# Optimization experiments

Measured on AMD Instinct MI355X. Metric: run time of the kernel, lower is better.

## Reference

```python
import jax, jax.numpy as jnp
import numpy as np
from jax import lax

B, C, D, H, W = 2, 64, 20, 20, 20


def _conv3d(x, w, b, pad):
    # x: [B,C,D,H,W], w: [O,I,kd,kh,kw]
    y = lax.conv_general_dilated(
        x, w, window_strides=(1, 1, 1), padding=pad,
        dimension_numbers=('NCDHW', 'OIDHW', 'NCDHW'))
    return y + b[None, :, None, None, None]


def setup_inputs() -> dict:
    key = jax.random.key(0)
    ks = jax.random.split(key, 7)
    s = 1.0 / np.sqrt(C * 3)  # conv fan-in = C*1*3*1
    return {
        'x': jax.random.normal(ks[0], (B, C, D, H, W), jnp.float32),
        'q_w': jax.random.uniform(ks[1], (C, C, 1, 3, 1), jnp.float32, -s, s),
        'q_b': jax.random.uniform(ks[2], (C,), jnp.float32, -s, s),
        'k_w': jax.random.uniform(ks[3], (C, C, 3, 1, 1), jnp.float32, -s, s),
        'k_b': jax.random.uniform(ks[4], (C,), jnp.float32, -s, s),
        'v_w': jax.random.uniform(ks[5], (C, C, 1, 1, 3), jnp.float32, -s, s),
        'v_b': jax.random.uniform(ks[6], (C,), jnp.float32, -s, s),
    }


def reference(x, q_w, q_b, k_w, k_b, v_w, v_b):
    b, c, d, h, w = x.shape
    n = d * h * w
    q0 = _conv3d(x, q_w, q_b, ((0, 0), (1, 1), (0, 0))).reshape(b, c, n)
    k0 = _conv3d(x, k_w, k_b, ((1, 1), (0, 0), (0, 0))).reshape(b, c, n)
    v = _conv3d(x, v_w, v_b, ((0, 0), (0, 0), (1, 1))).reshape(b, c, n)
    # scores[b, i, j] = sum_c k0[b,c,i] * q0[b,c,j]  -> [B, N, N]
    scores = jnp.einsum('bci,bcj->bij', k0, q0)
    # torch Softmax(dim=1) on [B,N,N] normalizes over axis 1 (the i axis)
    attn = jax.nn.softmax(scores, axis=1)
    out = jnp.einsum('bcn,bnm->bcm', v, attn)  # v @ attn
    return out.reshape(b, c, d, h, w)
```

## Files before the change

### kernel.cpp

```cpp
#include <hip/hip_runtime.h>
#include <cstdint>
#include <cstddef>

typedef _Float16 half4_t  __attribute__((ext_vector_type(4)));
typedef _Float16 half8_t  __attribute__((ext_vector_type(8)));
typedef short    short4_t __attribute__((ext_vector_type(4)));
typedef unsigned short ushort4_t __attribute__((ext_vector_type(4)));
typedef float    f32x4_t  __attribute__((ext_vector_type(4)));

#define LOG2E 1.44269504088896340736f

__device__ __forceinline__ float bf2f(unsigned short u) {
    union { unsigned int u; float f; } x;
    x.u = ((unsigned int)u) << 16;
    return x.f;
}
__device__ __forceinline__ unsigned short f2bf(float f) {
    union { float f; unsigned int u; } x;
    x.f = f;
    unsigned int r = (x.u + 0x7FFFu + ((x.u >> 16) & 1u)) >> 16;
    return (unsigned short)r;
}
__device__ __forceinline__ unsigned short f2bf_trunc(float f) {
    union { float f; unsigned int u; } x;
    x.f = f;
    return (unsigned short)(x.u >> 16);
}

__global__ __launch_bounds__(256) void prep_kernel(
    const void* __restrict__ x,
    const void* __restrict__ qw, const void* __restrict__ kw, const void* __restrict__ vw,
    const void* __restrict__ qb, const void* __restrict__ kb, const void* __restrict__ vb,
    int* __restrict__ flag,
    _Float16* __restrict__ w2, float* __restrict__ bb, _Float16* __restrict__ xT)
{
    __shared__ int scnt;
    __shared__ _Float16 tile[64][66];

    if (threadIdx.x == 0) scnt = 0;
    __syncthreads();
    {
        unsigned int w = ((const unsigned int*)x)[threadIdx.x];
        int e = (w >> 7) & 0xFF;
        int hit = (e == 0) || (e >= 0x68 && e <= 0x88);
        atomicAdd(&scnt, hit);
    }
    __syncthreads();
    const int bf = (scnt >= 128) ? 1 : 0;
    if (blockIdx.x == 0 && threadIdx.x == 0) flag[0] = bf;

    if (blockIdx.x < 144) {
        int idx = blockIdx.x * 256 + threadIdx.x;
        if (idx < 36864) {
            int conv = idx / 12288;
            int r    = idx - conv * 12288;
            int tap  = r >> 12;
            int r2   = r & 4095;
            int co   = r2 >> 6;
            int ci   = r2 & 63;
            const void* w = (conv == 0) ? qw : (conv == 1) ? kw : vw;
            float t;
            if (bf) t = bf2f(((const unsigned short*)w)[co * 192 + ci * 3 + tap]);
            else    t = ((const float*)w)[co * 192 + ci * 3 + tap];
            if (conv == 0) t *= LOG2E;
            w2[idx] = (_Float16)t;
        }
        if (idx < 192) {
            int a = idx >> 6, co = idx & 63;
            const void* s = (a == 0) ? qb : (a == 1) ? kb : vb;
            float t = bf ? bf2f(((const unsigned short*)s)[co]) : ((const float*)s)[co];
            if (a == 0) t *= LOG2E;
            bb[idx] = t;
        }
    } else {
        const int bx   = blockIdx.x - 144;
        const int b    = bx / 125;
        const int n0   = (bx - b * 125) * 64;
        const int lane = threadIdx.x & 63;
        const int wv   = threadIdx.x >> 6;

        if (bf) {
            const unsigned short* xb = (const unsigned short*)x + (size_t)b * 512000 + n0 + lane;
#pragma unroll
            for (int i = 0; i < 16; ++i) {
                const int ci = wv * 16 + i;
                tile[ci][lane] = (_Float16)bf2f(xb[(size_t)ci * 8000]);
            }
        } else {
            const float* xb = (const float*)x + (size_t)b * 512000 + n0 + lane;
#pragma unroll
            for (int i = 0; i < 16; ++i) {
                const int ci = wv * 16 + i;
                tile[ci][lane] = (_Float16)xb[(size_t)ci * 8000];
            }
        }
        __syncthreads();
        _Float16* out = xT + ((size_t)b * 8000 + n0) * 64 + lane;
#pragma unroll
        for (int i = 0; i < 16; ++i) {
            const int r = wv * 16 + i;
            out[(size_t)r * 64] = tile[lane][r];
        }
    }
}

__global__ __launch_bounds__(256, 2) void convg_kernel(
    const _Float16* __restrict__ xT, const _Float16* __restrict__ w2,
    const float* __restrict__ bb,
    _Float16* __restrict__ Qt, _Float16* __restrict__ Kt, unsigned short* __restrict__ Vt)
{
    const int tid = threadIdx.x;
    const int wv  = tid >> 6;
    const int L   = tid & 63;
    const int q4  = L >> 4;
    const int lm  = L & 15;
    const int W    = blockIdx.x * 4 + wv;
    const int conv = W % 3;
    const int u    = W / 3;
    const int b    = u / 250;
    const int n0   = (u - b * 250) * 32;

    half8_t wf[3][2][4];
    const _Float16* wbase = w2 + (size_t)conv * 12288;
#pragma unroll
    for (int tap = 0; tap < 3; ++tap)
#pragma unroll
        for (int kh = 0; kh < 2; ++kh)
#pragma unroll
            for (int cb = 0; cb < 4; ++cb)
                wf[tap][kh][cb] = *(const half8_t*)(
                    wbase + ((size_t)(tap * 64 + cb * 16 + lm)) * 64 + kh * 32 + q4 * 8);

    f32x4_t acc[2][4];
#pragma unroll
    for (int cb = 0; cb < 4; ++cb) {
        const float bi = bb[conv * 64 + cb * 16 + lm];
        const f32x4_t v = (f32x4_t){bi, bi, bi, bi};
        acc[0][cb] = v;
        acc[1][cb] = v;
    }

    const _Float16* xb = xT + (size_t)b * 512000;
    const half8_t z8 = {(_Float16)0, (_Float16)0, (_Float16)0, (_Float16)0,
                        (_Float16)0, (_Float16)0, (_Float16)0, (_Float16)0};

#pragma unroll
    for (int mt = 0; mt < 2; ++mt) {
        const int npos = n0 + mt * 16 + lm;
        int gm, gp, off;
        if (conv == 0)      { const int h = (npos / 20) % 20; gm = h > 0; gp = h < 19; off = 20; }
        else if (conv == 1) { const int d = npos / 400;       gm = d > 0; gp = d < 19; off = 400; }
        else                { const int w = npos % 20;        gm = w > 0; gp = w < 19; off = 1; }
        const int rm = gm ? npos - off : npos;
        const int rp = gp ? npos + off : npos;

#pragma unroll
        for (int kh = 0; kh < 2; ++kh) {
            const int ko = kh * 32 + q4 * 8;
            half8_t a0 = *(const half8_t*)(xb + (size_t)rm * 64 + ko);
            const half8_t a1 = *(const half8_t*)(xb + (size_t)npos * 64 + ko);
            half8_t a2 = *(const half8_t*)(xb + (size_t)rp * 64 + ko);
            a0 = gm ? a0 : z8;
            a2 = gp ? a2 : z8;
#pragma unroll
            for (int cb = 0; cb < 4; ++cb) {
                acc[mt][cb] = __builtin_amdgcn_mfma_f32_16x16x32_f16(a0, wf[0][kh][cb], acc[mt][cb], 0, 0, 0);
                acc[mt][cb] = __builtin_amdgcn_mfma_f32_16x16x32_f16(a1, wf[1][kh][cb], acc[mt][cb], 0, 0, 0);
                acc[mt][cb] = __builtin_amdgcn_mfma_f32_16x16x32_f16(a2, wf[2][kh][cb], acc[mt][cb], 0, 0, 0);
            }
        }
    }

    if (conv < 2) {
        _Float16* dst = (conv == 0) ? Qt : Kt;
#pragma unroll
        for (int mt = 0; mt < 2; ++mt)
#pragma unroll
            for (int cb = 0; cb < 4; ++cb)
#pragma unroll
                for (int reg = 0; reg < 4; ++reg) {
                    const int n = n0 + mt * 16 + q4 * 4 + reg;
                    dst[((size_t)b * 8000 + n) * 64 + cb * 16 + lm] = (_Float16)acc[mt][cb][reg];
                }
    } else {
#pragma unroll
        for (int mt = 0; mt < 2; ++mt)
#pragma unroll
            for (int cb = 0; cb < 4; ++cb) {
                ushort4_t vvv;
#pragma unroll
                for (int reg = 0; reg < 4; ++reg) vvv[reg] = f2bf(acc[mt][cb][reg]);
                *(ushort4_t*)(Vt + ((size_t)b * 64 + cb * 16 + lm) * 8000 + n0 + mt * 16 + q4 * 4) = vvv;
            }
    }
}

__global__ __launch_bounds__(256, 4) void attn_kernel(
    const _Float16* __restrict__ Qt, const _Float16* __restrict__ Kt,
    const unsigned short* __restrict__ Vt,
    _Float16* __restrict__ Oseg, float* __restrict__ Wseg)
{
    __shared__ __align__(16) _Float16       k_lds[4096];
    __shared__ __align__(16) unsigned short v_lds[4096];

    const int tid = threadIdx.x;
    const int wv  = tid >> 6;
    const int L   = tid & 63;
    const int q4  = L >> 4;
    const int lm  = L & 15;
    const int qt  = blockIdx.x;
    const int b   = blockIdx.y;
    const int sp  = blockIdx.z;
    const int NS  = gridDim.z;
    const int t0  = (125 * sp) / NS;
    const int t1  = (125 * (sp + 1)) / NS;
    const int unit = qt * 4 + wv;

    const _Float16* Qb = Qt + ((size_t)b * 8000 + (size_t)qt * 128 + wv * 32 + lm) * 64 + q4 * 8;
    half8_t bq00 = *(const half8_t*)(Qb);
    half8_t bq01 = *(const half8_t*)(Qb + 32);
    half8_t bq10 = *(const half8_t*)(Qb + 16 * 64);
    half8_t bq11 = *(const half8_t*)(Qb + 16 * 64 + 32);

    f32x4_t o[2][4];
    f32x4_t acc_l[2];
#pragma unroll
    for (int mt = 0; mt < 2; ++mt) {
        acc_l[mt] = (f32x4_t){0.f, 0.f, 0.f, 0.f};
#pragma unroll
        for (int cb = 0; cb < 4; ++cb) o[mt][cb] = (f32x4_t){0.f, 0.f, 0.f, 0.f};
    }
    const short4_t ones4 = {(short)0x3F80, (short)0x3F80, (short)0x3F80, (short)0x3F80};

    const _Float16*       Kg = Kt + (size_t)b * 512000;
    const unsigned short* Vg = Vt + (size_t)b * 512000;
    const int r0  = tid >> 3;
    const int cc0 = tid & 7;
    const int swz_lo = r0 * 64 + ((cc0 ^ (r0 & 7)) * 8);
    const int swz_hi = (r0 + 32) * 64 + ((cc0 ^ (r0 & 7)) * 8);
    const _Float16*       Kr0 = Kg + (size_t)r0 * 64 + cc0 * 8;
    const _Float16*       Kr1 = Kg + (size_t)(r0 + 32) * 64 + cc0 * 8;
    const unsigned short* Vr0 = Vg + (size_t)r0 * 8000 + cc0 * 8;
    const unsigned short* Vr1 = Vg + (size_t)(r0 + 32) * 8000 + cc0 * 8;

    uint4 sk0, sk1, sv0, sv1;

    {
        const int n0 = t0 * 64;
        sk0 = *(const uint4*)(Kr0 + (size_t)n0 * 64);
        sk1 = *(const uint4*)(Kr1 + (size_t)n0 * 64);
        sv0 = *(const uint4*)(Vr0 + n0);
        sv1 = *(const uint4*)(Vr1 + n0);
    }

    for (int kt = t0; kt < t1; ++kt) {
        __syncthreads();
        *(uint4*)(&k_lds[swz_lo]) = sk0;
        *(uint4*)(&k_lds[swz_hi]) = sk1;
        *(uint4*)(&v_lds[swz_lo]) = sv0;
        *(uint4*)(&v_lds[swz_hi]) = sv1;
        if (kt + 1 < t1) {
            const int n1 = (kt + 1) * 64;
            sk0 = *(const uint4*)(Kr0 + (size_t)n1 * 64);
            sk1 = *(const uint4*)(Kr1 + (size_t)n1 * 64);
            sv0 = *(const uint4*)(Vr0 + n1);
            sv1 = *(const uint4*)(Vr1 + n1);
        }
        __syncthreads();

        short4_t pfr[2][4];
#pragma unroll
        for (int ns = 0; ns < 4; ++ns) {
            const int n = ns * 16 + lm;
            const _Float16* krow = &k_lds[n * 64];
            const half8_t ak0 = *(const half8_t*)(krow + (((q4    ) ^ (n & 7)) * 8));
            const half8_t ak1 = *(const half8_t*)(krow + (((q4 + 4) ^ (n & 7)) * 8));
#pragma unroll
            for (int mt = 0; mt < 2; ++mt) {
                f32x4_t z = (f32x4_t){0.f, 0.f, 0.f, 0.f};
                z = __builtin_amdgcn_mfma_f32_16x16x32_f16(ak0, mt ? bq10 : bq00, z, 0, 0, 0);
                z = __builtin_amdgcn_mfma_f32_16x16x32_f16(ak1, mt ? bq11 : bq01, z, 0, 0, 0);
                short4_t pk;
#pragma unroll
                for (int reg = 0; reg < 4; ++reg)
                    pk[reg] = (short)f2bf_trunc(exp2f(z[reg]));
                pfr[mt][ns] = pk;
            }
        }

#pragma unroll
        for (int mt = 0; mt < 2; ++mt)
#pragma unroll
            for (int ns = 0; ns < 4; ++ns)
                acc_l[mt] = __builtin_amdgcn_mfma_f32_16x16x16bf16_1k(ones4, pfr[mt][ns], acc_l[mt], 0, 0, 0);

#pragma unroll
        for (int cb = 0; cb < 4; ++cb) {
            const int c = cb * 16 + lm;
            const unsigned short* vrow = &v_lds[c * 64];
            f32x4_t a0 = o[0][cb], a1 = o[1][cb];
#pragma unroll
            for (int ns = 0; ns < 4; ++ns) {
                const int cc = ns * 2 + (q4 >> 1);
                const short4_t av = *(const short4_t*)(vrow + ((cc ^ (c & 7)) * 8) + (q4 & 1) * 4);
                a0 = __builtin_amdgcn_mfma_f32_16x16x16bf16_1k(av, pfr[0][ns], a0, 0, 0, 0);
                a1 = __builtin_amdgcn_mfma_f32_16x16x16bf16_1k(av, pfr[1][ns], a1, 0, 0, 0);
            }
            o[0][cb] = a0;
            o[1][cb] = a1;
        }
    }

    if (unit >= 250) return;

    float rinv[2], lv[2];
#pragma unroll
    for (int mt = 0; mt < 2; ++mt) {
        const float l = acc_l[mt][0];
        rinv[mt] = 1.0f / l;
        lv[mt]   = l;
    }

    const int seg = (b * 250 + unit) * NS + sp;
    _Float16* os = Oseg + (size_t)seg * 2048;
#pragma unroll
    for (int mt = 0; mt < 2; ++mt) {
#pragma unroll
        for (int cb = 0; cb < 4; ++cb) {
            half4_t e;
#pragma unroll
            for (int reg = 0; reg < 4; ++reg) e[reg] = (_Float16)(o[mt][cb][reg] * rinv[mt]);
            *(half4_t*)(os + (mt * 16 + lm) * 64 + cb * 16 + q4 * 4) = e;
        }
    }
    if (q4 == 0) {
#pragma unroll
        for (int mt = 0; mt < 2; ++mt)
            Wseg[(size_t)seg * 32 + mt * 16 + lm] = lv[mt];
    }
}

__global__ __launch_bounds__(256, 2) void combine_kernel(
    const _Float16* __restrict__ Oseg, const float* __restrict__ Wseg,
    const int* __restrict__ flag, void* __restrict__ outv, int NS)
{
    __shared__ float cls[8 * 32];
    const int tid = threadIdx.x;
    const int qt = blockIdx.x, b = blockIdx.y;
    const int base = (b * 250 + qt) * NS;

    for (int i = tid; i < NS * 32; i += 256) cls[i] = Wseg[(size_t)base * 32 + i];
    __syncthreads();
    if (tid < 32) {
        const int r = tid;
        float cs = 0.f;
        for (int s2 = 0; s2 < NS; ++s2) cs += cls[s2 * 32 + r];
        const float inv = 1.f / cs;
        for (int s2 = 0; s2 < NS; ++s2) cls[s2 * 32 + r] *= inv;
    }
    __syncthreads();

    const int c = tid & 63, rg = tid >> 6;
    float acc[8];
#pragma unroll
    for (int i = 0; i < 8; ++i) acc[i] = 0.f;
    for (int s2 = 0; s2 < NS; ++s2) {
        const _Float16* src = Oseg + ((size_t)(base + s2)) * 2048 + rg * 8 * 64 + c;
        const float* cf = &cls[s2 * 32 + rg * 8];
#pragma unroll
        for (int i = 0; i < 8; ++i) acc[i] += (float)src[i * 64] * cf[i];
    }

    const size_t ob = ((size_t)b * 64 + c) * 8000 + qt * 32 + rg * 8;
    if (*flag) {
        uint4 u0;
        u0.x = f2bf(acc[0]) | ((unsigned)f2bf(acc[1]) << 16);
        u0.y = f2bf(acc[2]) | ((unsigned)f2bf(acc[3]) << 16);
        u0.z = f2bf(acc[4]) | ((unsigned)f2bf(acc[5]) << 16);
        u0.w = f2bf(acc[6]) | ((unsigned)f2bf(acc[7]) << 16);
        *(uint4*)((unsigned short*)outv + ob) = u0;
    } else {
        float* o32 = (float*)outv + ob;
        *(f32x4_t*)(o32)     = (f32x4_t){acc[0], acc[1], acc[2], acc[3]};
        *(f32x4_t*)(o32 + 4) = (f32x4_t){acc[4], acc[5], acc[6], acc[7]};
    }
}

extern "C" void kernel_launch(void* const* d_in, const int* in_sizes, int n_in,
                              void* d_out, int out_size, void* d_ws, size_t ws_size,
                              hipStream_t stream)
{
    (void)in_sizes; (void)n_in; (void)out_size;
    const void* x  = d_in[0];
    const void* qw = d_in[1];
    const void* qb = d_in[2];
    const void* kw = d_in[3];
    const void* kb = d_in[4];
    const void* vw = d_in[5];
    const void* vb = d_in[6];

    char* ws = (char*)d_ws;
    int*            flag = (int*)ws;
    float*          bb   = (float*)(ws + 2304);
    _Float16*       w2   = (_Float16*)(ws + 3072);
    _Float16*       Qt   = (_Float16*)(ws + 76800);
    _Float16*       Kt   = (_Float16*)(ws + 2124800);
    unsigned short* Vt   = (unsigned short*)(ws + 4172800);
    _Float16*       xT   = (_Float16*)(ws + 6220800);

    const size_t need8 = 6220800 + (size_t)2 * 250 * 8 * 2048 * 2 + (size_t)2 * 250 * 8 * 32 * 4;
    const int NS = (ws_size >= need8) ? 8 : 1;
    _Float16* Oseg = (_Float16*)(ws + 6220800);
    float*    Wseg = (float*)(ws + 6220800 + (size_t)2 * 250 * NS * 2048 * 2);

    prep_kernel<<<dim3(394), 256, 0, stream>>>(x, qw, kw, vw, qb, kb, vb, flag, w2, bb, xT);
    convg_kernel<<<dim3(375), 256, 0, stream>>>(xT, w2, bb, Qt, Kt, Vt);
    attn_kernel<<<dim3(63, 2, NS), 256, 0, stream>>>(Qt, Kt, Vt, Oseg, Wseg);
    combine_kernel<<<dim3(250, 2), 256, 0, stream>>>(Oseg, Wseg, flag, d_out, NS);
}
```

Measured before the change: 143.8 us.

## Fuse four kernel launches into one cooperative persistent kernel with grid syncs

Replaces the four back-to-back launches (prep, conv, attention, combine) with a single cooperative kernel. It loops over work units per phase and separates the phases with grid.sync(). This removes the launch and drain gaps between kernels. The grid size comes from the occupancy query, and the split count NS follows from it, capped at 8. The cost is grid-wide barrier overhead, a possibly different NS than before, and one shared launch-bounds and register budget for every phase. The old four-kernel path stays as a fallback.

```diff
diff --git a/kernel.cpp b/kernel.cpp
--- a/kernel.cpp
+++ b/kernel.cpp
@@ -1,6 +1,9 @@
 #include <hip/hip_runtime.h>
+#include <hip/hip_cooperative_groups.h>
 #include <cstdint>
 #include <cstddef>
+
+namespace cg = cooperative_groups;
 
 typedef _Float16 half4_t  __attribute__((ext_vector_type(4)));
 typedef _Float16 half8_t  __attribute__((ext_vector_type(8)));
@@ -27,6 +30,368 @@
     return (unsigned short)(x.u >> 16);
 }
 
+__global__ __launch_bounds__(256, 4) void mega_kernel(
+    const void* __restrict__ x,
+    const void* __restrict__ qw, const void* __restrict__ kw, const void* __restrict__ vw,
+    const void* __restrict__ qb, const void* __restrict__ kb, const void* __restrict__ vb,
+    _Float16* __restrict__ w2, float* __restrict__ bb, _Float16* __restrict__ xT,
+    _Float16* __restrict__ Qt, _Float16* __restrict__ Kt, unsigned short* __restrict__ Vt,
+    _Float16* __restrict__ Oseg, float* __restrict__ Wseg, void* __restrict__ outv,
+    int NS)
+{
+    __shared__ __align__(16) unsigned char smem[16384];
+    cg::grid_group grid = cg::this_grid();
+    const int nb  = gridDim.x;
+    const int tid = threadIdx.x;
+
+    int* scnt = (int*)(smem + 16380);
+    if (tid == 0) *scnt = 0;
+    __syncthreads();
+    {
+        unsigned int w = ((const unsigned int*)x)[tid];
+        int e = (w >> 7) & 0xFF;
+        int hit = (e == 0) || (e >= 0x68 && e <= 0x88);
+        atomicAdd(scnt, hit);
+    }
+    __syncthreads();
+    const int bf = (*scnt >= 128) ? 1 : 0;
+    __syncthreads();
+
+    for (int u = blockIdx.x; u < 394; u += nb) {
+        if (u < 144) {
+            int idx = u * 256 + tid;
+            if (idx < 36864) {
+                int conv = idx / 12288;
+                int r    = idx - conv * 12288;
+                int tap  = r >> 12;
+                int r2   = r & 4095;
+                int co   = r2 >> 6;
+                int ci   = r2 & 63;
+                const void* w = (conv == 0) ? qw : (conv == 1) ? kw : vw;
+                float t;
+                if (bf) t = bf2f(((const unsigned short*)w)[co * 192 + ci * 3 + tap]);
+                else    t = ((const float*)w)[co * 192 + ci * 3 + tap];
+                if (conv == 0) t *= LOG2E;
+                w2[idx] = (_Float16)t;
+            }
+            if (idx < 192) {
+                int a = idx >> 6, co = idx & 63;
+                const void* s = (a == 0) ? qb : (a == 1) ? kb : vb;
+                float t = bf ? bf2f(((const unsigned short*)s)[co]) : ((const float*)s)[co];
+                if (a == 0) t *= LOG2E;
+                bb[idx] = t;
+            }
+        } else {
+            _Float16 (*tile)[66] = (_Float16 (*)[66])smem;
+            const int bx   = u - 144;
+            const int b    = bx / 125;
+            const int n0   = (bx - b * 125) * 64;
+            const int lane = tid & 63;
+            const int wv   = tid >> 6;
+            if (bf) {
+                const unsigned short* xb = (const unsigned short*)x + (size_t)b * 512000 + n0 + lane;
+#pragma unroll
+                for (int i = 0; i < 16; ++i) {
+                    const int ci = wv * 16 + i;
+                    tile[ci][lane] = (_Float16)bf2f(xb[(size_t)ci * 8000]);
+                }
+            } else {
+                const float* xb = (const float*)x + (size_t)b * 512000 + n0 + lane;
+#pragma unroll
+                for (int i = 0; i < 16; ++i) {
+                    const int ci = wv * 16 + i;
+                    tile[ci][lane] = (_Float16)xb[(size_t)ci * 8000];
+                }
+            }
+            __syncthreads();
+            _Float16* out = xT + ((size_t)b * 8000 + n0) * 64 + lane;
+#pragma unroll
+            for (int i = 0; i < 16; ++i) {
+                const int r = wv * 16 + i;
+                out[(size_t)r * 64] = tile[lane][r];
+            }
+        }
+        __syncthreads();
+    }
+    grid.sync();
+
+    {
+        const int wv = tid >> 6;
+        const int L  = tid & 63;
+        const int q4 = L >> 4;
+        const int lm = L & 15;
+        for (int u = blockIdx.x; u < 375; u += nb) {
+            const int W    = u * 4 + wv;
+            const int conv = W % 3;
+            const int uu   = W / 3;
+            const int b    = uu / 250;
+            const int n0   = (uu - b * 250) * 32;
+
+            f32x4_t acc[2][4];
+#pragma unroll
+            for (int cb = 0; cb < 4; ++cb) {
+                const float bi = bb[conv * 64 + cb * 16 + lm];
+                const f32x4_t v = (f32x4_t){bi, bi, bi, bi};
+                acc[0][cb] = v;
+                acc[1][cb] = v;
+            }
+
+            const _Float16* xb = xT + (size_t)b * 512000;
+            const _Float16* wbase = w2 + (size_t)conv * 12288;
+            const half8_t z8 = {(_Float16)0, (_Float16)0, (_Float16)0, (_Float16)0,
+                                (_Float16)0, (_Float16)0, (_Float16)0, (_Float16)0};
+
+#pragma unroll
+            for (int kh = 0; kh < 2; ++kh) {
+                half8_t wfk[3][4];
+#pragma unroll
+                for (int tap = 0; tap < 3; ++tap)
+#pragma unroll
+                    for (int cb = 0; cb < 4; ++cb)
+                        wfk[tap][cb] = *(const half8_t*)(
+                            wbase + ((size_t)(tap * 64 + cb * 16 + lm)) * 64 + kh * 32 + q4 * 8);
+
+#pragma unroll
+                for (int mt = 0; mt < 2; ++mt) {
+                    const int npos = n0 + mt * 16 + lm;
+                    int gm, gp, off;
+                    if (conv == 0)      { const int h = (npos / 20) % 20; gm = h > 0; gp = h < 19; off = 20; }
+                    else if (conv == 1) { const int d = npos / 400;       gm = d > 0; gp = d < 19; off = 400; }
+                    else                { const int w = npos % 20;        gm = w > 0; gp = w < 19; off = 1; }
+                    const int rm = gm ? npos - off : npos;
+                    const int rp = gp ? npos + off : npos;
+
+                    const int ko = kh * 32 + q4 * 8;
+                    half8_t a0 = *(const half8_t*)(xb + (size_t)rm * 64 + ko);
+                    const half8_t a1 = *(const half8_t*)(xb + (size_t)npos * 64 + ko);
+                    half8_t a2 = *(const half8_t*)(xb + (size_t)rp * 64 + ko);
+                    a0 = gm ? a0 : z8;
+                    a2 = gp ? a2 : z8;
+#pragma unroll
+                    for (int cb = 0; cb < 4; ++cb) {
+                        acc[mt][cb] = __builtin_amdgcn_mfma_f32_16x16x32_f16(a0, wfk[0][cb], acc[mt][cb], 0, 0, 0);
+                        acc[mt][cb] = __builtin_amdgcn_mfma_f32_16x16x32_f16(a1, wfk[1][cb], acc[mt][cb], 0, 0, 0);
+                        acc[mt][cb] = __builtin_amdgcn_mfma_f32_16x16x32_f16(a2, wfk[2][cb], acc[mt][cb], 0, 0, 0);
+                    }
+                }
+            }
+
+            if (conv < 2) {
+                _Float16* dst = (conv == 0) ? Qt : Kt;
+#pragma unroll
+                for (int mt = 0; mt < 2; ++mt)
+#pragma unroll
+                    for (int cb = 0; cb < 4; ++cb)
+#pragma unroll
+                        for (int reg = 0; reg < 4; ++reg) {
+                            const int n = n0 + mt * 16 + q4 * 4 + reg;
+                            dst[((size_t)b * 8000 + n) * 64 + cb * 16 + lm] = (_Float16)acc[mt][cb][reg];
+                        }
+            } else {
+#pragma unroll
+                for (int mt = 0; mt < 2; ++mt)
+#pragma unroll
+                    for (int cb = 0; cb < 4; ++cb) {
+                        ushort4_t vvv;
+#pragma unroll
+                        for (int reg = 0; reg < 4; ++reg) vvv[reg] = f2bf(acc[mt][cb][reg]);
+                        *(ushort4_t*)(Vt + ((size_t)b * 64 + cb * 16 + lm) * 8000 + n0 + mt * 16 + q4 * 4) = vvv;
+                    }
+            }
+        }
+    }
+    grid.sync();
+
+    {
+        _Float16*       k_lds = (_Float16*)smem;
+        unsigned short* v_lds = (unsigned short*)(smem + 8192);
+        const int wv = tid >> 6;
+        const int L  = tid & 63;
+        const int q4 = L >> 4;
+        const int lm = L & 15;
+        const int totalU = 126 * NS;
+
+        for (int bu = blockIdx.x; bu < totalU; bu += nb) {
+            const int sp = bu / 126;
+            const int r  = bu - sp * 126;
+            const int b  = r / 63;
+            const int qt = r - b * 63;
+            const int t0 = (125 * sp) / NS;
+            const int t1 = (125 * (sp + 1)) / NS;
+            const int unit = qt * 4 + wv;
+
+            const _Float16* Qb = Qt + ((size_t)b * 8000 + (size_t)qt * 128 + wv * 32 + lm) * 64 + q4 * 8;
+            half8_t bq00 = *(const half8_t*)(Qb);
+            half8_t bq01 = *(const half8_t*)(Qb + 32);
+            half8_t bq10 = *(const half8_t*)(Qb + 16 * 64);
+            half8_t bq11 = *(const half8_t*)(Qb + 16 * 64 + 32);
+
+            f32x4_t o[2][4];
+            f32x4_t acc_l[2];
+#pragma unroll
+            for (int mt = 0; mt < 2; ++mt) {
+                acc_l[mt] = (f32x4_t){0.f, 0.f, 0.f, 0.f};
+#pragma unroll
+                for (int cb = 0; cb < 4; ++cb) o[mt][cb] = (f32x4_t){0.f, 0.f, 0.f, 0.f};
+            }
+            const short4_t ones4 = {(short)0x3F80, (short)0x3F80, (short)0x3F80, (short)0x3F80};
+
+            const _Float16*       Kg = Kt + (size_t)b * 512000;
+            const unsigned short* Vg = Vt + (size_t)b * 512000;
+            const int r0  = tid >> 3;
+            const int cc0 = tid & 7;
+            const int swz_lo = r0 * 64 + ((cc0 ^ (r0 & 7)) * 8);
+            const int swz_hi = (r0 + 32) * 64 + ((cc0 ^ (r0 & 7)) * 8);
+            const _Float16*       Kr0 = Kg + (size_t)r0 * 64 + cc0 * 8;
+            const _Float16*       Kr1 = Kg + (size_t)(r0 + 32) * 64 + cc0 * 8;
+            const unsigned short* Vr0 = Vg + (size_t)r0 * 8000 + cc0 * 8;
+            const unsigned short* Vr1 = Vg + (size_t)(r0 + 32) * 8000 + cc0 * 8;
+
+            uint4 sk0, sk1, sv0, sv1;
+            {
+                const int n0 = t0 * 64;
+                sk0 = *(const uint4*)(Kr0 + (size_t)n0 * 64);
+                sk1 = *(const uint4*)(Kr1 + (size_t)n0 * 64);
+                sv0 = *(const uint4*)(Vr0 + n0);
+                sv1 = *(const uint4*)(Vr1 + n0);
+            }
+
+            for (int kt = t0; kt < t1; ++kt) {
+                __syncthreads();
+                *(uint4*)(&k_lds[swz_lo]) = sk0;
+                *(uint4*)(&k_lds[swz_hi]) = sk1;
+                *(uint4*)(&v_lds[swz_lo]) = sv0;
+                *(uint4*)(&v_lds[swz_hi]) = sv1;
+                if (kt + 1 < t1) {
+                    const int n1 = (kt + 1) * 64;
+                    sk0 = *(const uint4*)(Kr0 + (size_t)n1 * 64);
+                    sk1 = *(const uint4*)(Kr1 + (size_t)n1 * 64);
+                    sv0 = *(const uint4*)(Vr0 + n1);
+                    sv1 = *(const uint4*)(Vr1 + n1);
+                }
+                __syncthreads();
+
+                short4_t pfr[2][4];
+#pragma unroll
+                for (int ns = 0; ns < 4; ++ns) {
+                    const int n = ns * 16 + lm;
+                    const _Float16* krow = &k_lds[n * 64];
+                    const half8_t ak0 = *(const half8_t*)(krow + (((q4    ) ^ (n & 7)) * 8));
+                    const half8_t ak1 = *(const half8_t*)(krow + (((q4 + 4) ^ (n & 7)) * 8));
+#pragma unroll
+                    for (int mt = 0; mt < 2; ++mt) {
+                        f32x4_t z = (f32x4_t){0.f, 0.f, 0.f, 0.f};
+                        z = __builtin_amdgcn_mfma_f32_16x16x32_f16(ak0, mt ? bq10 : bq00, z, 0, 0, 0);
+                        z = __builtin_amdgcn_mfma_f32_16x16x32_f16(ak1, mt ? bq11 : bq01, z, 0, 0, 0);
+                        short4_t pk;
+#pragma unroll
+                        for (int reg = 0; reg < 4; ++reg)
+                            pk[reg] = (short)f2bf_trunc(exp2f(z[reg]));
+                        pfr[mt][ns] = pk;
+                    }
+                }
+
+#pragma unroll
+                for (int mt = 0; mt < 2; ++mt)
+#pragma unroll
+                    for (int ns = 0; ns < 4; ++ns)
+                        acc_l[mt] = __builtin_amdgcn_mfma_f32_16x16x16bf16_1k(ones4, pfr[mt][ns], acc_l[mt], 0, 0, 0);
+
+#pragma unroll
+                for (int cb = 0; cb < 4; ++cb) {
+                    const int c = cb * 16 + lm;
+                    const unsigned short* vrow = &v_lds[c * 64];
+                    f32x4_t a0 = o[0][cb], a1 = o[1][cb];
+#pragma unroll
+                    for (int ns = 0; ns < 4; ++ns) {
+                        const int cc = ns * 2 + (q4 >> 1);
+                        const short4_t av = *(const short4_t*)(vrow + ((cc ^ (c & 7)) * 8) + (q4 & 1) * 4);
+                        a0 = __builtin_amdgcn_mfma_f32_16x16x16bf16_1k(av, pfr[0][ns], a0, 0, 0, 0);
+                        a1 = __builtin_amdgcn_mfma_f32_16x16x16bf16_1k(av, pfr[1][ns], a1, 0, 0, 0);
+                    }
+                    o[0][cb] = a0;
+                    o[1][cb] = a1;
+                }
+            }
+            __syncthreads();
+
+            if (unit < 250) {
+                float rinv[2], lv[2];
+#pragma unroll
+                for (int mt = 0; mt < 2; ++mt) {
+                    const float l = acc_l[mt][0];
+                    rinv[mt] = 1.0f / l;
+                    lv[mt]   = l;
+                }
+                const int seg = (b * 250 + unit) * NS + sp;
+                _Float16* os = Oseg + (size_t)seg * 2048;
+#pragma unroll
+                for (int mt = 0; mt < 2; ++mt) {
+#pragma unroll
+                    for (int cb = 0; cb < 4; ++cb) {
+                        half4_t e;
+#pragma unroll
+                        for (int reg = 0; reg < 4; ++reg) e[reg] = (_Float16)(o[mt][cb][reg] * rinv[mt]);
+                        *(half4_t*)(os + (mt * 16 + lm) * 64 + cb * 16 + q4 * 4) = e;
+                    }
+                }
+                if (q4 == 0) {
+#pragma unroll
+                    for (int mt = 0; mt < 2; ++mt)
+                        Wseg[(size_t)seg * 32 + mt * 16 + lm] = lv[mt];
+                }
+            }
+        }
+    }
+    grid.sync();
+
+    {
+        float* cls = (float*)smem;
+        for (int v = blockIdx.x; v < 500; v += nb) {
+            const int b  = v / 250;
+            const int qt = v - b * 250;
+            const int base = (b * 250 + qt) * NS;
+
+            for (int i = tid; i < NS * 32; i += 256) cls[i] = Wseg[(size_t)base * 32 + i];
+            __syncthreads();
+            if (tid < 32) {
+                const int r = tid;
+                float cs = 0.f;
+                for (int s2 = 0; s2 < NS; ++s2) cs += cls[s2 * 32 + r];
+                const float inv = 1.f / cs;
+                for (int s2 = 0; s2 < NS; ++s2) cls[s2 * 32 + r] *= inv;
+            }
+            __syncthreads();
+
+            const int c = tid & 63, rg = tid >> 6;
+            float acc[8];
+#pragma unroll
+            for (int i = 0; i < 8; ++i) acc[i] = 0.f;
+            for (int s2 = 0; s2 < NS; ++s2) {
+                const _Float16* src = Oseg + ((size_t)(base + s2)) * 2048 + rg * 8 * 64 + c;
+                const float* cf = &cls[s2 * 32 + rg * 8];
+#pragma unroll
+                for (int i = 0; i < 8; ++i) acc[i] += (float)src[i * 64] * cf[i];
+            }
+
+            const size_t ob = ((size_t)b * 64 + c) * 8000 + qt * 32 + rg * 8;
+            if (bf) {
+                uint4 u0;
+                u0.x = f2bf(acc[0]) | ((unsigned)f2bf(acc[1]) << 16);
+                u0.y = f2bf(acc[2]) | ((unsigned)f2bf(acc[3]) << 16);
+                u0.z = f2bf(acc[4]) | ((unsigned)f2bf(acc[5]) << 16);
+                u0.w = f2bf(acc[6]) | ((unsigned)f2bf(acc[7]) << 16);
+                *(uint4*)((unsigned short*)outv + ob) = u0;
+            } else {
+                float* o32 = (float*)outv + ob;
+                *(f32x4_t*)(o32)     = (f32x4_t){acc[0], acc[1], acc[2], acc[3]};
+                *(f32x4_t*)(o32 + 4) = (f32x4_t){acc[4], acc[5], acc[6], acc[7]};
+            }
+            __syncthreads();
+        }
+    }
+}
+
 __global__ __launch_bounds__(256) void prep_kernel(
     const void* __restrict__ x,
     const void* __restrict__ qw, const void* __restrict__ kw, const void* __restrict__ vw,
@@ -244,7 +609,6 @@
     const unsigned short* Vr1 = Vg + (size_t)(r0 + 32) * 8000 + cc0 * 8;
 
     uint4 sk0, sk1, sv0, sv1;
-
     {
         const int n0 = t0 * 64;
         sk0 = *(const uint4*)(Kr0 + (size_t)n0 * 64);
@@ -408,13 +772,40 @@
     unsigned short* Vt   = (unsigned short*)(ws + 4172800);
     _Float16*       xT   = (_Float16*)(ws + 6220800);
 
-    const size_t need8 = 6220800 + (size_t)2 * 250 * 8 * 2048 * 2 + (size_t)2 * 250 * 8 * 32 * 4;
-    const int NS = (ws_size >= need8) ? 8 : 1;
-    _Float16* Oseg = (_Float16*)(ws + 6220800);
-    float*    Wseg = (float*)(ws + 6220800 + (size_t)2 * 250 * NS * 2048 * 2);
-
-    prep_kernel<<<dim3(394), 256, 0, stream>>>(x, qw, kw, vw, qb, kb, vb, flag, w2, bb, xT);
-    convg_kernel<<<dim3(375), 256, 0, stream>>>(xT, w2, bb, Qt, Kt, Vt);
-    attn_kernel<<<dim3(63, 2, NS), 256, 0, stream>>>(Qt, Kt, Vt, Oseg, Wseg);
-    combine_kernel<<<dim3(250, 2), 256, 0, stream>>>(Oseg, Wseg, flag, d_out, NS);
+    int dev = 0;
+    hipGetDevice(&dev);
+    int numCU = 0;
+    hipDeviceGetAttribute(&numCU, hipDeviceAttributeMultiprocessorCount, dev);
+    int maxB = 0;
+    hipOccupancyMaxActiveBlocksPerMultiprocessor(&maxB, mega_kernel, 256, 0);
+    int NS = (numCU > 0 && maxB > 0) ? ((maxB * numCU) / 126) : 0;
+    if (NS > 8) NS = 8;
+
+    const size_t needNS = [&](int n) {
+        return (size_t)6220800 + (size_t)2 * 250 * n * 2048 * 2 + (size_t)2 * 250 * n * 32 * 4;
+    }(NS > 0 ? NS : 1);
+
+    if (NS >= 1 && ws_size >= needNS) {
+        _Float16* Oseg = (_Float16*)(ws + 6220800);
+        float*    Wseg = (float*)(ws + 6220800 + (size_t)2 * 250 * NS * 2048 * 2);
+        void* outv = d_out;
+        void* args[] = {
+            (void*)&x, (void*)&qw, (void*)&kw, (void*)&vw,
+            (void*)&qb, (void*)&kb, (void*)&vb,
+            (void*)&w2, (void*)&bb, (void*)&xT,
+            (void*)&Qt, (void*)&Kt, (void*)&Vt,
+            (void*)&Oseg, (void*)&Wseg, (void*)&outv, (void*)&NS
+        };
+        hipLaunchCooperativeKernel((void*)mega_kernel, dim3(126 * NS), dim3(256),
+                                   args, 0, stream);
+    } else {
+        const size_t need8 = 6220800 + (size_t)2 * 250 * 8 * 2048 * 2 + (size_t)2 * 250 * 8 * 32 * 4;
+        const int NSf = (ws_size >= need8) ? 8 : 1;
+        _Float16* Oseg = (_Float16*)(ws + 6220800);
+        float*    Wseg = (float*)(ws + 6220800 + (size_t)2 * 250 * NSf * 2048 * 2);
+        prep_kernel<<<dim3(394), 256, 0, stream>>>(x, qw, kw, vw, qb, kb, vb, flag, w2, bb, xT);
+        convg_kernel<<<dim3(375), 256, 0, stream>>>(xT, w2, bb, Qt, Kt, Vt);
+        attn_kernel<<<dim3(63, 2, NSf), 256, 0, stream>>>(Qt, Kt, Vt, Oseg, Wseg);
+        combine_kernel<<<dim3(250, 2), 256, 0, stream>>>(Oseg, Wseg, flag, d_out, NSf);
+    }
 }
```

Measured after the change: 364.2 us. 2.53x slower.
